# Kernel tuning notes

Measured on AMD Instinct MI355X. Metric: run time of the kernel, lower is better.

## Reference

```python
import jax, jax.numpy as jnp
import numpy as np

N_NODES = 100000
N_EDGES = 1600000
D_IN, D_HID, D_LAT = 128, 128, 64


def setup_inputs() -> dict:
    key = jax.random.key(0)
    ks = jax.random.split(key, 8)
    x = jax.random.normal(ks[0], (N_NODES, D_IN), dtype=jnp.float32)
    edge_index = jax.random.randint(ks[1], (2, N_EDGES), 0, N_NODES, dtype=jnp.int64)
    s1 = 1.0 / np.sqrt(D_IN)
    s2 = 1.0 / np.sqrt(D_HID)
    return {
        "x": x,
        "edge_index": edge_index,
        "W1_l": jax.random.normal(ks[2], (D_IN, D_HID), dtype=jnp.float32) * s1,
        "W1_r": jax.random.normal(ks[3], (D_IN, D_HID), dtype=jnp.float32) * s1,
        "b1": jnp.zeros((D_HID,), dtype=jnp.float32),
        "W2_l": jax.random.normal(ks[4], (D_HID, D_LAT), dtype=jnp.float32) * s2,
        "W2_r": jax.random.normal(ks[5], (D_HID, D_LAT), dtype=jnp.float32) * s2,
        "b2": jnp.zeros((D_LAT,), dtype=jnp.float32),
    }


def _sage_conv_mean(x, src, dst, W_l, W_r, b):
    """PyG SAGEConv with mean aggregation: lin_l(mean_j x_j) + lin_r(x_i)."""
    n = x.shape[0]
    # scatter-mean of source features into destination nodes
    agg = jax.ops.segment_sum(x[src], dst, num_segments=n)           # [N, d]
    deg = jax.ops.segment_sum(jnp.ones_like(dst, dtype=x.dtype), dst, num_segments=n)
    mean = agg / jnp.maximum(deg, 1.0)[:, None]
    return mean @ W_l + b + x @ W_r


def reference(x, edge_index, W1_l, W1_r, b1, W2_l, W2_r, b2):
    src, dst = edge_index[0], edge_index[1]
    h = jax.nn.relu(_sage_conv_mean(x, src, dst, W1_l, W1_r, b1))
    # Dropout(p=0.2) is identity in eval mode
    z = jax.nn.relu(_sage_conv_mean(h, src, dst, W2_l, W2_r, b2))
    return z
```

## Files before the change

### kernel.cpp

```cpp
#include <hip/hip_runtime.h>

#define N_NODES 100000
#define N_EDGES 1600000
#define D_IN 128
#define D_HID 128
#define D_LAT 64

#define BSHIFT 8
#define NB 392
#define CAP 4608
#define EPB 4096
#define PART_BLOCKS ((N_EDGES + EPB - 1) / EPB)
#define CVT_BLOCKS (((long)N_NODES * 128 / 16 + 255) / 256)

typedef unsigned short ushort_t;
typedef unsigned int uint_t;
typedef unsigned char uchar_t;
using bf16x8 = __attribute__((ext_vector_type(8))) short;
using f32x4  = __attribute__((ext_vector_type(4))) float;
using f32x2  = __attribute__((ext_vector_type(2))) float;

__device__ inline ushort_t f2bf(float f) {
    uint_t u = __float_as_uint(f);
    return (ushort_t)((u + 0x7fffu + ((u >> 16) & 1u)) >> 16);
}
__device__ inline uint_t pack2bf(float a, float b) {
    return (uint_t)f2bf(a) | ((uint_t)f2bf(b) << 16);
}
__device__ inline float bf2f(ushort_t u) {
    return __uint_as_float(((uint_t)u) << 16);
}

#if __has_builtin(__builtin_amdgcn_cvt_pk_f32_fp8) && __has_builtin(__builtin_amdgcn_cvt_pk_fp8_f32)
#define HW_FP8 1
template<bool HI>
__device__ inline f32x2 fp8pk2f(uint_t v) {
    return __builtin_amdgcn_cvt_pk_f32_fp8(v, HI);
}
__device__ inline uint_t f2fp8pk4(float a, float b, float c, float d) {
    uint_t w = __builtin_amdgcn_cvt_pk_fp8_f32(a, b, 0, false);
    w = __builtin_amdgcn_cvt_pk_fp8_f32(c, d, w, true);
    return w;
}
__device__ inline uchar_t f2fp8_byte(float f) {
    return (uchar_t)(__builtin_amdgcn_cvt_pk_fp8_f32(f, f, 0, false) & 0xff);
}
#else
__device__ inline float fp8b2f(uint_t b) {
    uint_t em = b & 0x7f;
    if (em == 0) return 0.f;
    uint_t bits = ((em << 20) + (120u << 23)) | ((b & 0x80u) << 24);
    return __uint_as_float(bits);
}
template<bool HI>
__device__ inline f32x2 fp8pk2f(uint_t v) {
    uint_t w = HI ? (v >> 16) : v;
    f32x2 r; r.x = fp8b2f(w & 0xff); r.y = fp8b2f((w >> 8) & 0xff);
    return r;
}
__device__ inline uint_t f2fp8_1(float f) {
    uint_t u = __float_as_uint(f);
    uint_t s = (u >> 31) << 7;
    uint_t au = u & 0x7fffffff;
    if (au >= 0x43e00000u) return s | 0x7e;
    if (au < 0x3c000000u) return s;
    uint_t r = au + 0x0007ffffu + ((au >> 20) & 1u);
    return s | (((r >> 20) - (120u << 3)) & 0x7f);
}
__device__ inline uint_t f2fp8pk4(float a, float b, float c, float d) {
    return f2fp8_1(a) | (f2fp8_1(b) << 8) | (f2fp8_1(c) << 16) | (f2fp8_1(d) << 24);
}
__device__ inline uchar_t f2fp8_byte(float f) { return (uchar_t)f2fp8_1(f); }
#endif

__device__ inline void accf8x4(float* a, uint_t w, int base) {
    f32x2 p0 = fp8pk2f<false>(w);
    f32x2 p1 = fp8pk2f<true>(w);
    a[base + 0] += p0.x; a[base + 1] += p0.y;
    a[base + 2] += p1.x; a[base + 3] += p1.y;
}
__device__ inline void accf8x16(float* a, uint4 u) {
    accf8x4(a, u.x, 0); accf8x4(a, u.y, 4); accf8x4(a, u.z, 8); accf8x4(a, u.w, 12);
}

template<int RSHIFT, int NV, int DEPTH, int STRIDE = 1>
__device__ inline void gather_acc_fp8n(const uchar_t* __restrict__ base,
                                       const int* __restrict__ idxp,
                                       int n, float* acc) {
    int k = 0;
    int idx[DEPTH];
    if (n >= DEPTH) {
        #pragma unroll
        for (int j = 0; j < DEPTH; ++j) idx[j] = idxp[j * STRIDE];
    }
    while (k + DEPTH <= n) {
        uint4 u[DEPTH][NV];
        #pragma unroll
        for (int j = 0; j < DEPTH; ++j) {
            #pragma unroll
            for (int v = 0; v < NV; ++v)
                u[j][v] = *(const uint4*)(base + ((long)idx[j] << RSHIFT) + v * 16);
        }
        int kn = k + DEPTH;
        if (kn + DEPTH <= n) {
            #pragma unroll
            for (int j = 0; j < DEPTH; ++j) idx[j] = idxp[(kn + j) * STRIDE];
        }
        #pragma unroll
        for (int j = 0; j < DEPTH; ++j) {
            #pragma unroll
            for (int v = 0; v < NV; ++v)
                accf8x16(acc + v * 16, u[j][v]);
        }
        k = kn;
    }
    if (k < n) {
        int m = n - k;
        int idr[DEPTH];
        #pragma unroll
        for (int j = 0; j < DEPTH; ++j) {
            int kk = k + j; if (kk > n - 1) kk = n - 1;
            idr[j] = idxp[kk * STRIDE];
        }
        uint4 u[DEPTH][NV];
        #pragma unroll
        for (int j = 0; j < DEPTH; ++j) {
            #pragma unroll
            for (int v = 0; v < NV; ++v)
                u[j][v] = *(const uint4*)(base + ((long)idr[j] << RSHIFT) + v * 16);
        }
        #pragma unroll
        for (int j = 0; j < DEPTH; ++j) {
            if (j < m) {
                #pragma unroll
                for (int v = 0; v < NV; ++v)
                    accf8x16(acc + v * 16, u[j][v]);
            }
        }
    }
}

__device__ inline void pack_w256(const float* Wl, const float* Wr, ushort_t* pack,
                                 int N, int tid) {
    int lane = tid & 63;
    int t = tid >> 6;
    int kt = t & 7;
    int nt = t >> 3;
    int n = nt * 16 + (lane & 15);
    int kbase = kt * 32 + (lane >> 4) * 8;
    ushort_t v[8];
    #pragma unroll
    for (int j = 0; j < 8; ++j) {
        int k = kbase + j;
        float w = (k < 128) ? Wl[k * N + n] : Wr[(k - 128) * N + n];
        v[j] = f2bf(w);
    }
    *(uint4*)(pack + (long)tid * 8) = *(uint4*)v;
}
__device__ inline void pack_w128(const float* W, ushort_t* pack, int N, int tid) {
    int lane = tid & 63;
    int t = tid >> 6;
    int kt = t & 3;
    int nt = t >> 2;
    int n = nt * 16 + (lane & 15);
    int kbase = kt * 32 + (lane >> 4) * 8;
    ushort_t v[8];
    #pragma unroll
    for (int j = 0; j < 8; ++j) v[j] = f2bf(W[(kbase + j) * N + n]);
    *(uint4*)(pack + (long)tid * 8) = *(uint4*)v;
}

__global__ __launch_bounds__(256) void prep_kernel(
        const float* __restrict__ W1_l, const float* __restrict__ W1_r,
        ushort_t* __restrict__ pack1,
        const float* __restrict__ W2_l, ushort_t* __restrict__ pack2l,
        const float* __restrict__ W2_r, ushort_t* __restrict__ pack2r,
        int* __restrict__ gCur,
        const float* __restrict__ x, ushort_t* __restrict__ xb,
        uchar_t* __restrict__ x8) {
    int b = blockIdx.x;
    if (b < 16) {
        pack_w256(W1_l, W1_r, pack1, 128, b * 256 + threadIdx.x);
    } else if (b < 20) {
        pack_w128(W2_l, pack2l, 64, (b - 16) * 256 + threadIdx.x);
    } else if (b < 24) {
        pack_w128(W2_r, pack2r, 64, (b - 20) * 256 + threadIdx.x);
    } else if (b < 26) {
        int t = (b - 24) * 256 + threadIdx.x;
        if (t < NB) gCur[t] = t * CAP;
    } else {
        long i = ((long)(b - 26) * 256 + threadIdx.x) * 16;
        if (i >= (long)N_NODES * 128) return;
        float4 a = *(const float4*)(x + i);
        float4 bb = *(const float4*)(x + i + 4);
        float4 c = *(const float4*)(x + i + 8);
        float4 d = *(const float4*)(x + i + 12);
        uint4 ob0, ob1;
        ob0.x = pack2bf(a.x, a.y);  ob0.y = pack2bf(a.z, a.w);
        ob0.z = pack2bf(bb.x, bb.y); ob0.w = pack2bf(bb.z, bb.w);
        ob1.x = pack2bf(c.x, c.y);  ob1.y = pack2bf(c.z, c.w);
        ob1.z = pack2bf(d.x, d.y);  ob1.w = pack2bf(d.z, d.w);
        *(uint4*)(xb + i) = ob0;
        *(uint4*)(xb + i + 8) = ob1;
        uint4 o8;
        o8.x = f2fp8pk4(a.x, a.y, a.z, a.w);
        o8.y = f2fp8pk4(bb.x, bb.y, bb.z, bb.w);
        o8.z = f2fp8pk4(c.x, c.y, c.z, c.w);
        o8.w = f2fp8pk4(d.x, d.y, d.z, d.w);
        *(uint4*)(x8 + i) = o8;
    }
}

__global__ __launch_bounds__(256) void bucket_scatter_kernel(const int* __restrict__ src,
                                                             const int* __restrict__ dst,
                                                             int* __restrict__ gCur,
                                                             int* __restrict__ bedges) {
    __shared__ int h[NB];
    __shared__ int start[NB];
    for (int j = threadIdx.x; j < NB; j += 256) h[j] = 0;
    __syncthreads();
    long base = (long)blockIdx.x * EPB + threadIdx.x * 16;
    int dc[16], sc[16];
    int cnt = 0;
    if (base + 16 <= N_EDGES) {
        #pragma unroll
        for (int j = 0; j < 4; ++j) {
            int4 d4 = *(const int4*)(dst + base + j * 4);
            int4 s4 = *(const int4*)(src + base + j * 4);
            dc[j * 4 + 0] = d4.x; dc[j * 4 + 1] = d4.y; dc[j * 4 + 2] = d4.z; dc[j * 4 + 3] = d4.w;
            sc[j * 4 + 0] = s4.x; sc[j * 4 + 1] = s4.y; sc[j * 4 + 2] = s4.z; sc[j * 4 + 3] = s4.w;
        }
        cnt = 16;
    } else if (base < N_EDGES) {
        cnt = (int)(N_EDGES - base);
        for (int j = 0; j < cnt; ++j) { dc[j] = dst[base + j]; sc[j] = src[base + j]; }
    }
    for (int j = 0; j < cnt; ++j) atomicAdd(&h[dc[j] >> BSHIFT], 1);
    __syncthreads();
    for (int j = threadIdx.x; j < NB; j += 256)
        start[j] = h[j] ? atomicAdd(&gCur[j], h[j]) : 0;
    __syncthreads();
    for (int j = 0; j < cnt; ++j) {
        int b = dc[j] >> BSHIFT;
        int p = atomicAdd(&start[b], 1);
        if (p < (b + 1) * CAP)
            bedges[p] = ((dc[j] & 255) << 24) | sc[j];
    }
}

__global__ __launch_bounds__(256) void bucket_sort_kernel(const int* __restrict__ gCur,
                                                          const int* __restrict__ bedges,
                                                          int* __restrict__ csr,
                                                          int2* __restrict__ off2) {
    __shared__ int sdata[256];
    __shared__ int cur[256];
    int b = blockIdx.x, t = threadIdx.x;
    int r0 = b * CAP;
    int n = gCur[b] - r0;
    if (n > CAP) n = CAP;
    cur[t] = 0;
    __syncthreads();
    for (int k = t * 4; k < n; k += 1024) {
        int4 v4 = *(const int4*)(bedges + r0 + k);
        int m = n - k;
        atomicAdd(&cur[(unsigned)v4.x >> 24], 1);
        if (m > 1) atomicAdd(&cur[(unsigned)v4.y >> 24], 1);
        if (m > 2) atomicAdd(&cur[(unsigned)v4.z >> 24], 1);
        if (m > 3) atomicAdd(&cur[(unsigned)v4.w >> 24], 1);
    }
    __syncthreads();
    int c = cur[t];
    sdata[t] = c;
    __syncthreads();
    for (int d = 1; d < 256; d <<= 1) {
        int u = (t >= d) ? sdata[t - d] : 0;
        __syncthreads();
        sdata[t] += u;
        __syncthreads();
    }
    int ex = (t == 0) ? 0 : sdata[t - 1];
    off2[(b << BSHIFT) + t] = make_int2(r0 + ex, c);
    cur[t] = ex;
    __syncthreads();
    for (int k = t * 4; k < n; k += 1024) {
        int4 v4 = *(const int4*)(bedges + r0 + k);
        int m = n - k;
        {
            int p = atomicAdd(&cur[(unsigned)v4.x >> 24], 1);
            csr[r0 + p] = v4.x & 0xFFFFFF;
        }
        if (m > 1) {
            int p = atomicAdd(&cur[(unsigned)v4.y >> 24], 1);
            csr[r0 + p] = v4.y & 0xFFFFFF;
        }
        if (m > 2) {
            int p = atomicAdd(&cur[(unsigned)v4.z >> 24], 1);
            csr[r0 + p] = v4.z & 0xFFFFFF;
        }
        if (m > 3) {
            int p = atomicAdd(&cur[(unsigned)v4.w >> 24], 1);
            csr[r0 + p] = v4.w & 0xFFFFFF;
        }
    }
}

#define HSTRIDE 132
__global__ __launch_bounds__(256) void mfma_mlp_fused_kernel(
        const int2* __restrict__ off2, const int* __restrict__ csr_src,
        const uchar_t* __restrict__ x8,
        const ushort_t* __restrict__ Ax,
        const ushort_t* __restrict__ pack1, const float* __restrict__ bias,
        const ushort_t* __restrict__ pack2l, const ushort_t* __restrict__ pack2r,
        ushort_t* __restrict__ f2, uchar_t* __restrict__ g8) {
    __shared__ ushort_t mtile[32 * HSTRIDE];
    __shared__ ushort_t htile[32 * HSTRIDE];
    long m0b = (long)blockIdx.x * 32;
    {
        int lane8 = threadIdx.x & 7;
        int local = threadIdx.x >> 3;
        long i = m0b + local;
        int2 bd = off2[i];
        const uchar_t* gbase = x8 + lane8 * 16;
        float acc[16];
        #pragma unroll
        for (int j = 0; j < 16; ++j) acc[j] = 0.f;
        gather_acc_fp8n<7, 1, 8>(gbase, csr_src + bd.x, bd.y, acc);
        float inv = (bd.y > 0) ? 1.f / (float)bd.y : 0.f;
        uint4 o0, o1;
        o0.x = pack2bf(acc[0] * inv,  acc[1] * inv);
        o0.y = pack2bf(acc[2] * inv,  acc[3] * inv);
        o0.z = pack2bf(acc[4] * inv,  acc[5] * inv);
        o0.w = pack2bf(acc[6] * inv,  acc[7] * inv);
        o1.x = pack2bf(acc[8] * inv,  acc[9] * inv);
        o1.y = pack2bf(acc[10] * inv, acc[11] * inv);
        o1.z = pack2bf(acc[12] * inv, acc[13] * inv);
        o1.w = pack2bf(acc[14] * inv, acc[15] * inv);
        ushort_t* mp = mtile + local * HSTRIDE + lane8 * 16;
        *(uint4*)mp = o0;
        *(uint4*)(mp + 8) = o1;
    }
    __syncthreads();
    int lane = threadIdx.x & 63;
    int wave = threadIdx.x >> 6;
    int wr = wave & 1;
    int wc = wave >> 1;
    int r = lane & 15;
    int quad = lane >> 4;
    int rowl = wr * 16 + r;
    long arow = m0b + rowl;

    bf16x8 areg[8];
    #pragma unroll
    for (int kt = 0; kt < 8; ++kt) {
        int k = (kt & 3) * 32 + quad * 8;
        areg[kt] = (kt < 4)
            ? *(const bf16x8*)(&mtile[rowl * HSTRIDE + k])
            : *(const bf16x8*)(Ax + arow * 128 + k);
    }

    f32x4 acc[4];
    #pragma unroll
    for (int nt = 0; nt < 4; ++nt) acc[nt] = (f32x4){0.f, 0.f, 0.f, 0.f};
    #pragma unroll
    for (int nt = 0; nt < 4; ++nt) {
        int gnt = wc * 4 + nt;
        #pragma unroll
        for (int kt = 0; kt < 8; ++kt) {
            bf16x8 bfrag = *(const bf16x8*)(pack1 + ((long)(gnt * 8 + kt) * 64 + lane) * 8);
            acc[nt] = __builtin_amdgcn_mfma_f32_16x16x32_bf16(areg[kt], bfrag, acc[nt], 0, 0, 0);
        }
    }

    #pragma unroll
    for (int nt = 0; nt < 4; ++nt) {
        int col = wc * 64 + nt * 16 + r;
        float bj = bias[col];
        #pragma unroll
        for (int q = 0; q < 4; ++q) {
            float v = fmaxf(acc[nt][q] + bj, 0.f);
            htile[(wr * 16 + quad * 4 + q) * HSTRIDE + col] = f2bf(v);
        }
    }
    __syncthreads();
    bf16x8 areg2[4];
    #pragma unroll
    for (int kt = 0; kt < 4; ++kt)
        areg2[kt] = *(const bf16x8*)(&htile[rowl * HSTRIDE + kt * 32 + quad * 8]);
    f32x4 gacc[2];
    #pragma unroll
    for (int nt = 0; nt < 2; ++nt) gacc[nt] = (f32x4){0.f, 0.f, 0.f, 0.f};
    #pragma unroll
    for (int nt = 0; nt < 2; ++nt) {
        int gnt = wc * 2 + nt;
        #pragma unroll
        for (int kt = 0; kt < 4; ++kt) {
            bf16x8 bfrag = *(const bf16x8*)(pack2l + ((long)(gnt * 4 + kt) * 64 + lane) * 8);
            gacc[nt] = __builtin_amdgcn_mfma_f32_16x16x32_bf16(areg2[kt], bfrag, gacc[nt], 0, 0, 0);
        }
    }
    #pragma unroll
    for (int nt = 0; nt < 2; ++nt) {
        int col = wc * 32 + nt * 16 + r;
        #pragma unroll
        for (int q = 0; q < 4; ++q) {
            long orow = m0b + wr * 16 + quad * 4 + q;
            g8[orow * 64 + col] = f2fp8_byte(gacc[nt][q]);
        }
    }
    f32x4 facc[2];
    #pragma unroll
    for (int nt = 0; nt < 2; ++nt) facc[nt] = (f32x4){0.f, 0.f, 0.f, 0.f};
    #pragma unroll
    for (int nt = 0; nt < 2; ++nt) {
        int gnt = wc * 2 + nt;
        #pragma unroll
        for (int kt = 0; kt < 4; ++kt) {
            bf16x8 bfrag = *(const bf16x8*)(pack2r + ((long)(gnt * 4 + kt) * 64 + lane) * 8);
            facc[nt] = __builtin_amdgcn_mfma_f32_16x16x32_bf16(areg2[kt], bfrag, facc[nt], 0, 0, 0);
        }
    }
    #pragma unroll
    for (int nt = 0; nt < 2; ++nt) {
        int col = wc * 32 + nt * 16 + r;
        #pragma unroll
        for (int q = 0; q < 4; ++q) {
            long orow = m0b + wr * 16 + quad * 4 + q;
            f2[orow * 64 + col] = f2bf(facc[nt][q]);
        }
    }
}

__global__ __launch_bounds__(256) void final_gather_kernel(
        const int2* __restrict__ off2, const int* __restrict__ csr_src,
        const uchar_t* __restrict__ g8,
        const ushort_t* __restrict__ f2, const float* __restrict__ b2,
        float* __restrict__ out) {
    int lane8 = threadIdx.x & 7;
    int d = lane8 & 3;
    int p = lane8 >> 2;
    int local = threadIdx.x >> 3;
    long i = (long)blockIdx.x * 32 + local;
    int2 bd = off2[i];
    int n = bd.y;
    const uchar_t* base = g8 + d * 16;
    float acc[16];
    #pragma unroll
    for (int j = 0; j < 16; ++j) acc[j] = 0.f;
    int np = (n + 1 - p) >> 1;
    gather_acc_fp8n<6, 1, 8, 2>(base, csr_src + bd.x + p, np, acc);
    #pragma unroll
    for (int j = 0; j < 16; ++j) acc[j] += __shfl_xor(acc[j], 4);
    float inv = (n > 0) ? 1.f / (float)n : 0.f;
    int dim0 = d * 16 + p * 8;
    ushort_t fu[8];
    *(uint4*)fu = *(const uint4*)(f2 + i * 64 + dim0);
    float o[8];
    #pragma unroll
    for (int j = 0; j < 8; ++j) {
        float m = bf2f(f2bf(acc[p * 8 + j] * inv));
        o[j] = fmaxf(m + bf2f(fu[j]) + b2[dim0 + j], 0.f);
    }
    *(float4*)(out + i * 64 + dim0)     = make_float4(o[0], o[1], o[2], o[3]);
    *(float4*)(out + i * 64 + dim0 + 4) = make_float4(o[4], o[5], o[6], o[7]);
}

extern "C" void kernel_launch(void* const* d_in, const int* in_sizes, int n_in,
                              void* d_out, int out_size, void* d_ws, size_t ws_size,
                              hipStream_t stream) {
    const float* x    = (const float*)d_in[0];
    const int*   ei   = (const int*)d_in[1];
    const float* W1_l = (const float*)d_in[2];
    const float* W1_r = (const float*)d_in[3];
    const float* b1   = (const float*)d_in[4];
    const float* W2_l = (const float*)d_in[5];
    const float* W2_r = (const float*)d_in[6];
    const float* b2   = (const float*)d_in[7];
    float* out = (float*)d_out;

    const int* src = ei;
    const int* dst = ei + N_EDGES;

    int*  gCur   = (int*)d_ws;
    int2* off2   = (int2*)(gCur + 512);
    int*  bedges = (int*)(off2 + 100608);
    int*  csr    = bedges + NB * CAP;
    ushort_t* xb = (ushort_t*)(csr + NB * CAP);
    uchar_t*  x8 = (uchar_t*)(xb + (long)N_NODES * 128);
    ushort_t* f2 = (ushort_t*)(x8 + (long)N_NODES * 128);
    ushort_t* pack1  = f2 + (long)N_NODES * 64;
    ushort_t* pack2l = pack1 + 256 * 128;
    ushort_t* pack2r = pack2l + 128 * 64;
    uchar_t*  g8     = (uchar_t*)(pack2r + 128 * 64);

    prep_kernel<<<26 + CVT_BLOCKS, 256, 0, stream>>>(
        W1_l, W1_r, pack1, W2_l, pack2l, W2_r, pack2r, gCur, x, xb, x8);

    bucket_scatter_kernel<<<PART_BLOCKS, 256, 0, stream>>>(src, dst, gCur, bedges);
    bucket_sort_kernel<<<NB, 256, 0, stream>>>(gCur, bedges, csr, off2);

    mfma_mlp_fused_kernel<<<N_NODES / 32, 256, 0, stream>>>(
        off2, csr, x8, xb, pack1, b1, pack2l, pack2r, f2, g8);

    final_gather_kernel<<<N_NODES / 32, 256, 0, stream>>>(
        off2, csr, g8, f2, b2, out);
}
```

Baseline: 229.1 us.

## Split layer-1 gather across thread pairs and shrink fused MLP tile to 16 rows

```diff
diff --git a/kernel.cpp b/kernel.cpp
--- a/kernel.cpp
+++ b/kernel.cpp
@@ -73,20 +73,18 @@
 __device__ inline uchar_t f2fp8_byte(float f) { return (uchar_t)f2fp8_1(f); }
 #endif
 
-__device__ inline void accf8x4(float* a, uint_t w, int base) {
-    f32x2 p0 = fp8pk2f<false>(w);
-    f32x2 p1 = fp8pk2f<true>(w);
-    a[base + 0] += p0.x; a[base + 1] += p0.y;
-    a[base + 2] += p1.x; a[base + 3] += p1.y;
-}
-__device__ inline void accf8x16(float* a, uint4 u) {
-    accf8x4(a, u.x, 0); accf8x4(a, u.y, 4); accf8x4(a, u.z, 8); accf8x4(a, u.w, 12);
+__device__ inline void accf8x4p(f32x2* a, uint_t w, int b2) {
+    a[b2]     += fp8pk2f<false>(w);
+    a[b2 + 1] += fp8pk2f<true>(w);
+}
+__device__ inline void accf8x16p(f32x2* a, uint4 u) {
+    accf8x4p(a, u.x, 0); accf8x4p(a, u.y, 2); accf8x4p(a, u.z, 4); accf8x4p(a, u.w, 6);
 }
 
 template<int RSHIFT, int NV, int DEPTH, int STRIDE = 1>
 __device__ inline void gather_acc_fp8n(const uchar_t* __restrict__ base,
                                        const int* __restrict__ idxp,
-                                       int n, float* acc) {
+                                       int n, f32x2* acc) {
     int k = 0;
     int idx[DEPTH];
     if (n >= DEPTH) {
@@ -110,7 +108,7 @@
         for (int j = 0; j < DEPTH; ++j) {
             #pragma unroll
             for (int v = 0; v < NV; ++v)
-                accf8x16(acc + v * 16, u[j][v]);
+                accf8x16p(acc + v * 8, u[j][v]);
         }
         k = kn;
     }
@@ -134,7 +132,7 @@
             if (j < m) {
                 #pragma unroll
                 for (int v = 0; v < NV; ++v)
-                    accf8x16(acc + v * 16, u[j][v]);
+                    accf8x16p(acc + v * 8, u[j][v]);
             }
         }
     }
@@ -312,58 +310,56 @@
         const ushort_t* __restrict__ pack1, const float* __restrict__ bias,
         const ushort_t* __restrict__ pack2l, const ushort_t* __restrict__ pack2r,
         ushort_t* __restrict__ f2, uchar_t* __restrict__ g8) {
-    __shared__ ushort_t mtile[32 * HSTRIDE];
-    __shared__ ushort_t htile[32 * HSTRIDE];
-    long m0b = (long)blockIdx.x * 32;
+    __shared__ ushort_t mtile[16 * HSTRIDE];
+    __shared__ ushort_t htile[16 * HSTRIDE];
+    long m0b = (long)blockIdx.x * 16;
     {
-        int lane8 = threadIdx.x & 7;
-        int local = threadIdx.x >> 3;
+        int lane16 = threadIdx.x & 15;
+        int d = lane16 & 7;
+        int p = lane16 >> 3;
+        int local = threadIdx.x >> 4;
         long i = m0b + local;
         int2 bd = off2[i];
-        const uchar_t* gbase = x8 + lane8 * 16;
-        float acc[16];
-        #pragma unroll
-        for (int j = 0; j < 16; ++j) acc[j] = 0.f;
-        gather_acc_fp8n<7, 1, 8>(gbase, csr_src + bd.x, bd.y, acc);
-        float inv = (bd.y > 0) ? 1.f / (float)bd.y : 0.f;
-        uint4 o0, o1;
-        o0.x = pack2bf(acc[0] * inv,  acc[1] * inv);
-        o0.y = pack2bf(acc[2] * inv,  acc[3] * inv);
-        o0.z = pack2bf(acc[4] * inv,  acc[5] * inv);
-        o0.w = pack2bf(acc[6] * inv,  acc[7] * inv);
-        o1.x = pack2bf(acc[8] * inv,  acc[9] * inv);
-        o1.y = pack2bf(acc[10] * inv, acc[11] * inv);
-        o1.z = pack2bf(acc[12] * inv, acc[13] * inv);
-        o1.w = pack2bf(acc[14] * inv, acc[15] * inv);
-        ushort_t* mp = mtile + local * HSTRIDE + lane8 * 16;
-        *(uint4*)mp = o0;
-        *(uint4*)(mp + 8) = o1;
+        int n = bd.y;
+        const uchar_t* gbase = x8 + d * 16;
+        f32x2 acc2[8];
+        #pragma unroll
+        for (int j = 0; j < 8; ++j) acc2[j] = (f32x2){0.f, 0.f};
+        int np = (n + 1 - p) >> 1;
+        gather_acc_fp8n<7, 1, 8, 2>(gbase, csr_src + bd.x + p, np, acc2);
+        float* pa = (float*)acc2;
+        #pragma unroll
+        for (int j = 0; j < 16; ++j) pa[j] += __shfl_xor(pa[j], 8);
+        float inv = (n > 0) ? 1.f / (float)n : 0.f;
+        int dim0 = d * 16 + p * 8;
+        uint_t o[4];
+        #pragma unroll
+        for (int j = 0; j < 4; ++j)
+            o[j] = pack2bf(pa[p * 8 + j * 2] * inv, pa[p * 8 + j * 2 + 1] * inv);
+        *(uint4*)(mtile + local * HSTRIDE + dim0) = *(uint4*)o;
     }
     __syncthreads();
     int lane = threadIdx.x & 63;
     int wave = threadIdx.x >> 6;
-    int wr = wave & 1;
-    int wc = wave >> 1;
     int r = lane & 15;
     int quad = lane >> 4;
-    int rowl = wr * 16 + r;
-    long arow = m0b + rowl;
+    long arow = m0b + r;
 
     bf16x8 areg[8];
     #pragma unroll
     for (int kt = 0; kt < 8; ++kt) {
         int k = (kt & 3) * 32 + quad * 8;
         areg[kt] = (kt < 4)
-            ? *(const bf16x8*)(&mtile[rowl * HSTRIDE + k])
+            ? *(const bf16x8*)(&mtile[r * HSTRIDE + k])
             : *(const bf16x8*)(Ax + arow * 128 + k);
     }
 
-    f32x4 acc[4];
-    #pragma unroll
-    for (int nt = 0; nt < 4; ++nt) acc[nt] = (f32x4){0.f, 0.f, 0.f, 0.f};
-    #pragma unroll
-    for (int nt = 0; nt < 4; ++nt) {
-        int gnt = wc * 4 + nt;
+    f32x4 acc[2];
+    #pragma unroll
+    for (int nt = 0; nt < 2; ++nt) acc[nt] = (f32x4){0.f, 0.f, 0.f, 0.f};
+    #pragma unroll
+    for (int nt = 0; nt < 2; ++nt) {
+        int gnt = wave * 2 + nt;
         #pragma unroll
         for (int kt = 0; kt < 8; ++kt) {
             bf16x8 bfrag = *(const bf16x8*)(pack1 + ((long)(gnt * 8 + kt) * 64 + lane) * 8);
@@ -372,60 +368,46 @@
     }
 
     #pragma unroll
-    for (int nt = 0; nt < 4; ++nt) {
-        int col = wc * 64 + nt * 16 + r;
+    for (int nt = 0; nt < 2; ++nt) {
+        int col = wave * 32 + nt * 16 + r;
         float bj = bias[col];
         #pragma unroll
         for (int q = 0; q < 4; ++q) {
             float v = fmaxf(acc[nt][q] + bj, 0.f);
-            htile[(wr * 16 + quad * 4 + q) * HSTRIDE + col] = f2bf(v);
+            htile[(quad * 4 + q) * HSTRIDE + col] = f2bf(v);
         }
     }
     __syncthreads();
     bf16x8 areg2[4];
     #pragma unroll
     for (int kt = 0; kt < 4; ++kt)
-        areg2[kt] = *(const bf16x8*)(&htile[rowl * HSTRIDE + kt * 32 + quad * 8]);
-    f32x4 gacc[2];
-    #pragma unroll
-    for (int nt = 0; nt < 2; ++nt) gacc[nt] = (f32x4){0.f, 0.f, 0.f, 0.f};
-    #pragma unroll
-    for (int nt = 0; nt < 2; ++nt) {
-        int gnt = wc * 2 + nt;
-        #pragma unroll
-        for (int kt = 0; kt < 4; ++kt) {
-            bf16x8 bfrag = *(const bf16x8*)(pack2l + ((long)(gnt * 4 + kt) * 64 + lane) * 8);
-            gacc[nt] = __builtin_amdgcn_mfma_f32_16x16x32_bf16(areg2[kt], bfrag, gacc[nt], 0, 0, 0);
-        }
-    }
-    #pragma unroll
-    for (int nt = 0; nt < 2; ++nt) {
-        int col = wc * 32 + nt * 16 + r;
+        areg2[kt] = *(const bf16x8*)(&htile[r * HSTRIDE + kt * 32 + quad * 8]);
+    f32x4 gacc = (f32x4){0.f, 0.f, 0.f, 0.f};
+    #pragma unroll
+    for (int kt = 0; kt < 4; ++kt) {
+        bf16x8 bfrag = *(const bf16x8*)(pack2l + ((long)(wave * 4 + kt) * 64 + lane) * 8);
+        gacc = __builtin_amdgcn_mfma_f32_16x16x32_bf16(areg2[kt], bfrag, gacc, 0, 0, 0);
+    }
+    {
+        int col = wave * 16 + r;
         #pragma unroll
         for (int q = 0; q < 4; ++q) {
-            long orow = m0b + wr * 16 + quad * 4 + q;
-            g8[orow * 64 + col] = f2fp8_byte(gacc[nt][q]);
-        }
-    }
-    f32x4 facc[2];
-    #pragma unroll
-    for (int nt = 0; nt < 2; ++nt) facc[nt] = (f32x4){0.f, 0.f, 0.f, 0.f};
-    #pragma unroll
-    for (int nt = 0; nt < 2; ++nt) {
-        int gnt = wc * 2 + nt;
-        #pragma unroll
-        for (int kt = 0; kt < 4; ++kt) {
-            bf16x8 bfrag = *(const bf16x8*)(pack2r + ((long)(gnt * 4 + kt) * 64 + lane) * 8);
-            facc[nt] = __builtin_amdgcn_mfma_f32_16x16x32_bf16(areg2[kt], bfrag, facc[nt], 0, 0, 0);
-        }
-    }
-    #pragma unroll
-    for (int nt = 0; nt < 2; ++nt) {
-        int col = wc * 32 + nt * 16 + r;
+            long orow = m0b + quad * 4 + q;
+            g8[orow * 64 + col] = f2fp8_byte(gacc[q]);
+        }
+    }
+    f32x4 facc = (f32x4){0.f, 0.f, 0.f, 0.f};
+    #pragma unroll
+    for (int kt = 0; kt < 4; ++kt) {
+        bf16x8 bfrag = *(const bf16x8*)(pack2r + ((long)(wave * 4 + kt) * 64 + lane) * 8);
+        facc = __builtin_amdgcn_mfma_f32_16x16x32_bf16(areg2[kt], bfrag, facc, 0, 0, 0);
+    }
+    {
+        int col = wave * 16 + r;
         #pragma unroll
         for (int q = 0; q < 4; ++q) {
-            long orow = m0b + wr * 16 + quad * 4 + q;
-            f2[orow * 64 + col] = f2bf(facc[nt][q]);
+            long orow = m0b + quad * 4 + q;
+            f2[orow * 64 + col] = f2bf(facc[q]);
         }
     }
 }
@@ -443,13 +425,14 @@
     int2 bd = off2[i];
     int n = bd.y;
     const uchar_t* base = g8 + d * 16;
-    float acc[16];
-    #pragma unroll
-    for (int j = 0; j < 16; ++j) acc[j] = 0.f;
+    f32x2 acc2[8];
+    #pragma unroll
+    for (int j = 0; j < 8; ++j) acc2[j] = (f32x2){0.f, 0.f};
     int np = (n + 1 - p) >> 1;
-    gather_acc_fp8n<6, 1, 8, 2>(base, csr_src + bd.x + p, np, acc);
-    #pragma unroll
-    for (int j = 0; j < 16; ++j) acc[j] += __shfl_xor(acc[j], 4);
+    gather_acc_fp8n<6, 1, 8, 2>(base, csr_src + bd.x + p, np, acc2);
+    float* pa = (float*)acc2;
+    #pragma unroll
+    for (int j = 0; j < 16; ++j) pa[j] += __shfl_xor(pa[j], 4);
     float inv = (n > 0) ? 1.f / (float)n : 0.f;
     int dim0 = d * 16 + p * 8;
     ushort_t fu[8];
@@ -457,7 +440,7 @@
     float o[8];
     #pragma unroll
     for (int j = 0; j < 8; ++j) {
-        float m = bf2f(f2bf(acc[p * 8 + j] * inv));
+        float m = bf2f(f2bf(pa[p * 8 + j] * inv));
         o[j] = fmaxf(m + bf2f(fu[j]) + b2[dim0 + j], 0.f);
     }
     *(float4*)(out + i * 64 + dim0)     = make_float4(o[0], o[1], o[2], o[3]);
@@ -498,7 +481,7 @@
     bucket_scatter_kernel<<<PART_BLOCKS, 256, 0, stream>>>(src, dst, gCur, bedges);
     bucket_sort_kernel<<<NB, 256, 0, stream>>>(gCur, bedges, csr, off2);
 
-    mfma_mlp_fused_kernel<<<N_NODES / 32, 256, 0, stream>>>(
+    mfma_mlp_fused_kernel<<<N_NODES / 16, 256, 0, stream>>>(
         off2, csr, x8, xb, pack1, b1, pack2l, pack2r, f2, g8);
 
     final_gather_kernel<<<N_NODES / 32, 256, 0, stream>>>(
```

Result: slower. 235.8 us (+2.9%).
